# Optimization experiments

Hardware: AMD Instinct MI355X
Metric: run time of the kernel (lower is better)

The kernel has to match this reference:

```python
import jax, jax.numpy as jnp
import numpy as np

D_MODEL = 1024
N_HEADS = 16
D_FF = 4 * D_MODEL
EPS = 1e-5


def _layer_norm(x, g, b):
    mu = jnp.mean(x, axis=-1, keepdims=True)
    var = jnp.mean(jnp.square(x - mu), axis=-1, keepdims=True)
    return (x - mu) * jax.lax.rsqrt(var + EPS) * g + b


def _mha(x, Wq, Wk, Wv, Wo, causal):
    B, S, D = x.shape
    H = N_HEADS
    Dh = D // H
    q = (x @ Wq).reshape(B, S, H, Dh)
    k = (x @ Wk).reshape(B, S, H, Dh)
    v = (x @ Wv).reshape(B, S, H, Dh)
    scores = jnp.einsum('bqhd,bkhd->bhqk', q, k) / jnp.sqrt(jnp.asarray(Dh, x.dtype))
    if causal:
        mask = jnp.tril(jnp.ones((S, S), dtype=bool))  # [S,S] causal mask
        scores = jnp.where(mask, scores, jnp.asarray(-1e9, x.dtype))
    attn = jax.nn.softmax(scores, axis=-1)
    out = jnp.einsum('bhqk,bkhd->bqhd', attn, v).reshape(B, S, D)
    return out @ Wo


def _ffn(x, W1, b1, W2, b2):
    return jax.nn.relu(x @ W1 + b1) @ W2 + b2


def setup_inputs() -> dict:
    key = jax.random.key(0)
    ks = jax.random.split(key, 12)
    sd = 1.0 / np.sqrt(D_MODEL)
    sf = 1.0 / np.sqrt(D_FF)
    B, S = 4, 1024
    return {
        'X': jax.random.normal(ks[0], (B, S, D_MODEL), jnp.float32),
        'Wq1': jax.random.normal(ks[1], (D_MODEL, D_MODEL), jnp.float32) * sd,
        'Wk1': jax.random.normal(ks[2], (D_MODEL, D_MODEL), jnp.float32) * sd,
        'Wv1': jax.random.normal(ks[3], (D_MODEL, D_MODEL), jnp.float32) * sd,
        'Wo1': jax.random.normal(ks[4], (D_MODEL, D_MODEL), jnp.float32) * sd,
        'Wq2': jax.random.normal(ks[5], (D_MODEL, D_MODEL), jnp.float32) * sd,
        'Wk2': jax.random.normal(ks[6], (D_MODEL, D_MODEL), jnp.float32) * sd,
        'Wv2': jax.random.normal(ks[7], (D_MODEL, D_MODEL), jnp.float32) * sd,
        'Wo2': jax.random.normal(ks[8], (D_MODEL, D_MODEL), jnp.float32) * sd,
        'ln_g': jnp.ones((D_MODEL,), jnp.float32),
        'ln_b': jnp.zeros((D_MODEL,), jnp.float32),
        'W1': jax.random.normal(ks[9], (D_MODEL, D_FF), jnp.float32) * sd,
        'b1': jnp.zeros((D_FF,), jnp.float32),
        'W2': jax.random.normal(ks[10], (D_FF, D_MODEL), jnp.float32) * sf,
        'b2': jnp.zeros((D_MODEL,), jnp.float32),
    }


def reference(X, Wq1, Wk1, Wv1, Wo1, Wq2, Wk2, Wv2, Wo2, ln_g, ln_b, W1, b1, W2, b2):
    # Faithful to the torch module (including its unusual residual wiring
    # and the single shared LayerNorm used at all three sites).
    masked = _mha(X, Wq1, Wk1, Wv1, Wo1, causal=True)
    norm_masked = X + _layer_norm(masked, ln_g, ln_b)
    attn2 = _mha(norm_masked, Wq2, Wk2, Wv2, Wo2, causal=False)
    norm_attn2 = attn2 + _layer_norm(attn2, ln_g, ln_b)
    ff = _ffn(norm_attn2, W1, b1, W2, b2)
    return norm_attn2 + _layer_norm(ff, ln_g, ln_b)
```

## Files before the change

### kernel.cpp

```cpp
#include <hip/hip_runtime.h>
#include <hip/hip_bf16.h>

#define D_MODEL 1024
#define N_HEADS 16
#define DH 64
#define D_FF   4096
#define SEQ    1024
#define BATCH  4
#define TOK    (BATCH*SEQ)
#define EPS    1e-5f
#define SCALE  0.125f
#define QSCL   0.18033688f

typedef unsigned short USHORT;
typedef __attribute__((ext_vector_type(8))) short short8v;
typedef __attribute__((ext_vector_type(4))) float f32x4;

__device__ __forceinline__ USHORT f2bf(float f) {
    unsigned int u; __builtin_memcpy(&u, &f, 4);
    u += 0x7fffu + ((u >> 16) & 1u);
    return (USHORT)(u >> 16);
}
__device__ __forceinline__ USHORT f2bf_fast(float f) {
    unsigned int u; __builtin_memcpy(&u, &f, 4);
    return (USHORT)((u + 0x8000u) >> 16);
}
__device__ __forceinline__ float bf2f(USHORT s) {
    unsigned int u = ((unsigned int)s) << 16;
    float f; __builtin_memcpy(&f, &u, 4);
    return f;
}
__device__ __forceinline__ float max3f(float a, float b, float c) {
    return fmaxf(fmaxf(a, b), c);
}

__device__ __forceinline__ short8v ld_frag(const USHORT* lds, int row, int c8) {
    return *reinterpret_cast<const short8v*>(
        &lds[row * 64 + (((c8) ^ (row & 7)) << 3)]);
}
__device__ __forceinline__ short8v ld128(const USHORT* lds, int row, int cu) {
    return *reinterpret_cast<const short8v*>(
        &lds[row * 128 + (((cu) ^ (row & 15)) << 3)]);
}

#define GLDS(gsrc, ldst) \
    __builtin_amdgcn_global_load_lds( \
        (const __attribute__((address_space(1))) void*)(gsrc), \
        (__attribute__((address_space(3))) void*)(ldst), 16, 0, 0)

#define WAITVM(n) asm volatile("s_waitcnt vmcnt(" #n ")" ::: "memory")

__global__ __launch_bounds__(512) void gemm_k256_kernel(
    const USHORT* __restrict__ A, const USHORT* __restrict__ Bt,
    float* __restrict__ Cf, USHORT* __restrict__ Cb, USHORT* __restrict__ Ck,
    USHORT* __restrict__ VtOut,
    int M, int N, int K, const float* __restrict__ bias, int relu, int qkv)
{
    __shared__ USHORT As[2][256 * 64];
    __shared__ USHORT Bs[2][256 * 64];

    const int tid = threadIdx.x;
    const int l   = tid & 63;
    const int w   = tid >> 6;
    const int wr  = w >> 2, wc = w & 3;
    const int lr  = l & 15, lg = l >> 4;

    const int gx  = gridDim.x;
    const int nwg = gx * gridDim.y;
    const int lin = blockIdx.y * gx + blockIdx.x;
    const int swz = (lin & 7) * (nwg >> 3) + (lin >> 3);
    const int m0  = (swz / gx) * 256, n0 = (swz % gx) * 256;

    const USHORT* aS[4]; const USHORT* bS[4]; int dOf[4];
#pragma unroll
    for (int p = 0; p < 4; ++p) {
        const int q = p * 512 + tid;
        const int row = q >> 3, cu = q & 7;
        const int cs = ((cu ^ (row & 7)) << 3);
        aS[p] = A  + (size_t)(m0 + row) * K + cs;
        bS[p] = Bt + (size_t)(n0 + row) * K + cs;
        dOf[p] = (p * 512 + w * 64) * 8;
    }

    auto stage = [&](int buf, int k0) {
#pragma unroll
        for (int p = 0; p < 4; ++p) {
            GLDS(aS[p] + k0, &As[buf][dOf[p]]);
            GLDS(bS[p] + k0, &Bs[buf][dOf[p]]);
        }
    };

    f32x4 acc[8][4];
#pragma unroll
    for (int i = 0; i < 8; ++i)
#pragma unroll
        for (int j = 0; j < 4; ++j) acc[i][j] = (f32x4){0.f, 0.f, 0.f, 0.f};

    const int nk = K >> 6;
    stage(0, 0);

    for (int t = 0; t < nk; ++t) {
        const int cur = t & 1;
        if (t + 1 < nk) {
            stage(cur ^ 1, (t + 1) << 6);
            WAITVM(8);
        } else {
            WAITVM(0);
        }
        __builtin_amdgcn_s_barrier();

#pragma unroll
        for (int ks = 0; ks < 2; ++ks) {
            short8v bfr[4];
#pragma unroll
            for (int ni = 0; ni < 4; ++ni)
                bfr[ni] = ld_frag(Bs[cur], wc * 64 + ni * 16 + lr, ks * 4 + lg);
            __builtin_amdgcn_s_setprio(1);
#pragma unroll
            for (int mi = 0; mi < 8; ++mi) {
                short8v af = ld_frag(As[cur], wr * 128 + mi * 16 + lr, ks * 4 + lg);
#pragma unroll
                for (int ni = 0; ni < 4; ++ni)
                    acc[mi][ni] = __builtin_amdgcn_mfma_f32_16x16x32_bf16(
                        af, bfr[ni], acc[mi][ni], 0, 0, 0);
            }
            __builtin_amdgcn_s_setprio(0);
        }
        __builtin_amdgcn_s_barrier();
    }

    if (qkv) {
#pragma unroll
        for (int mi = 0; mi < 8; ++mi) {
            const int row = m0 + wr * 128 + mi * 16 + (l >> 4) * 4;
#pragma unroll
            for (int ni = 0; ni < 4; ++ni) {
                const int col = n0 + wc * 64 + ni * 16 + lr;
                if (col < 2048) {
                    USHORT* dst = (col < 1024) ? Cb : Ck;
                    const float scl = (col < 1024) ? QSCL : 1.f;
                    const int c = col & 1023;
#pragma unroll
                    for (int j = 0; j < 4; ++j)
                        dst[(size_t)(row + j) * D_MODEL + c] =
                            f2bf(acc[mi][ni][j] * scl);
                } else {
                    const int c = col - 2048;
                    const int bb = row >> 10, jr = row & 1023;
                    const int hh = c >> 6, dd = c & 63;
                    ushort4 pk = make_ushort4(
                        f2bf(acc[mi][ni][0]), f2bf(acc[mi][ni][1]),
                        f2bf(acc[mi][ni][2]), f2bf(acc[mi][ni][3]));
                    *reinterpret_cast<ushort4*>(
                        &VtOut[((size_t)(bb * 16 + hh) * 64 + dd) * 1024 + jr]) = pk;
                }
            }
        }
    } else {
#pragma unroll
        for (int mi = 0; mi < 8; ++mi) {
            const int row = m0 + wr * 128 + mi * 16 + (l >> 4) * 4;
#pragma unroll
            for (int ni = 0; ni < 4; ++ni) {
                const int col = n0 + wc * 64 + ni * 16 + lr;
                const float bv = bias ? bias[col] : 0.f;
#pragma unroll
                for (int j = 0; j < 4; ++j) {
                    float v = acc[mi][ni][j] + bv;
                    if (relu) v = fmaxf(v, 0.f);
                    const size_t idx = (size_t)(row + j) * N + col;
                    if (Cf) Cf[idx] = v;
                    if (Cb) Cb[idx] = f2bf(v);
                }
            }
        }
    }
}

__global__ __launch_bounds__(512) void gemm_k128c_kernel(
    const USHORT* __restrict__ A, const USHORT* __restrict__ Bt,
    USHORT* __restrict__ Pa, USHORT* __restrict__ Pb,
    int M, int N, int K)
{
    __shared__ USHORT As[2][128 * 64];
    __shared__ USHORT Bs[2][128 * 64];

    const int tid = threadIdx.x;
    const int l   = tid & 63;
    const int w   = tid >> 6;
    const int wr  = w >> 2, wc = w & 3;
    const int lr  = l & 15, lg = l >> 4;

    const int gx  = gridDim.x;
    const int nwg = gx * gridDim.y;
    const int lin = blockIdx.y * gx + blockIdx.x;
    const int swz = (lin & 7) * (nwg >> 3) + (lin >> 3);
    const int my  = swz / gx;
    const int mt  = M >> 7;
    const int part = my / mt;
    const int m0  = (my % mt) << 7;
    const int n0  = (swz % gx) * 128;
    const int koff = part * (K >> 1);
    USHORT* dst = part ? Pb : Pa;

    const USHORT* aS[2]; const USHORT* bS[2]; int dOf[2];
#pragma unroll
    for (int p = 0; p < 2; ++p) {
        const int q = p * 512 + tid;
        const int row = q >> 3, cu = q & 7;
        const int cs = ((cu ^ (row & 7)) << 3);
        aS[p] = A  + (size_t)(m0 + row) * K + cs;
        bS[p] = Bt + (size_t)(n0 + row) * K + cs;
        dOf[p] = (p * 512 + w * 64) * 8;
    }

    auto stage = [&](int buf, int k0) {
#pragma unroll
        for (int p = 0; p < 2; ++p) {
            GLDS(aS[p] + k0, &As[buf][dOf[p]]);
            GLDS(bS[p] + k0, &Bs[buf][dOf[p]]);
        }
    };

    f32x4 acc[4][2];
#pragma unroll
    for (int i = 0; i < 4; ++i)
#pragma unroll
        for (int j = 0; j < 2; ++j) acc[i][j] = (f32x4){0.f, 0.f, 0.f, 0.f};

    const int nk = K >> 7;
    stage(0, koff);

    for (int t = 0; t < nk; ++t) {
        const int cur = t & 1;
        if (t + 1 < nk) {
            stage(cur ^ 1, koff + ((t + 1) << 6));
            WAITVM(4);
        } else {
            WAITVM(0);
        }
        __builtin_amdgcn_s_barrier();

#pragma unroll
        for (int ks = 0; ks < 2; ++ks) {
            short8v bfr[2];
#pragma unroll
            for (int ni = 0; ni < 2; ++ni)
                bfr[ni] = ld_frag(Bs[cur], wc * 32 + ni * 16 + lr, ks * 4 + lg);
            __builtin_amdgcn_s_setprio(1);
#pragma unroll
            for (int mi = 0; mi < 4; ++mi) {
                short8v af = ld_frag(As[cur], wr * 64 + mi * 16 + lr, ks * 4 + lg);
#pragma unroll
                for (int ni = 0; ni < 2; ++ni)
                    acc[mi][ni] = __builtin_amdgcn_mfma_f32_16x16x32_bf16(
                        af, bfr[ni], acc[mi][ni], 0, 0, 0);
            }
            __builtin_amdgcn_s_setprio(0);
        }
        __builtin_amdgcn_s_barrier();
    }

#pragma unroll
    for (int mi = 0; mi < 4; ++mi) {
        const int row = m0 + wr * 64 + mi * 16 + (l >> 4) * 4;
#pragma unroll
        for (int ni = 0; ni < 2; ++ni) {
            const int col = n0 + wc * 32 + ni * 16 + lr;
#pragma unroll
            for (int j = 0; j < 4; ++j)
                dst[(size_t)(row + j) * N + col] = f2bf(acc[mi][ni][j]);
        }
    }
}

struct TcvtB4 {
    const float* s0; const float* s1; const float* s2; const float* s3;
    USHORT* d0; USHORT* d1; USHORT* d2; USHORT* d3;
};

__device__ __forceinline__ void tcvt_body(
    const float* __restrict__ W, USHORT* __restrict__ Wt, int K, int N)
{
    __shared__ USHORT L[64][65];
    const int tid = threadIdx.x;
    const int tx = tid & 15, ty = tid >> 4;
    const int n0 = blockIdx.x * 64, k0 = blockIdx.y * 64;
#pragma unroll
    for (int r = 0; r < 4; ++r) {
        int kr = ty + 16 * r;
        float4 v = *reinterpret_cast<const float4*>(
            &W[(size_t)(k0 + kr) * N + n0 + tx * 4]);
        L[tx * 4 + 0][kr] = f2bf(v.x);
        L[tx * 4 + 1][kr] = f2bf(v.y);
        L[tx * 4 + 2][kr] = f2bf(v.z);
        L[tx * 4 + 3][kr] = f2bf(v.w);
    }
    __syncthreads();
#pragma unroll
    for (int r = 0; r < 4; ++r) {
        int nr = ty + 16 * r;
        ushort4 o = make_ushort4(L[nr][tx * 4 + 0], L[nr][tx * 4 + 1],
                                 L[nr][tx * 4 + 2], L[nr][tx * 4 + 3]);
        *reinterpret_cast<ushort4*>(&Wt[(size_t)(n0 + nr) * K + k0 + tx * 4]) = o;
    }
}

__global__ __launch_bounds__(256) void tcvt_kernel(
    const float* __restrict__ W, USHORT* __restrict__ Wt, int K, int N)
{
    tcvt_body(W, Wt, K, N);
}

__global__ __launch_bounds__(256) void tcvt4_kernel(TcvtB4 p, int K, int N)
{
    const int z = blockIdx.z;
    const float* W = (z == 0) ? p.s0 : (z == 1) ? p.s1 : (z == 2) ? p.s2 : p.s3;
    USHORT*    Wt = (z == 0) ? p.d0 : (z == 1) ? p.d1 : (z == 2) ? p.d2 : p.d3;
    tcvt_body(W, Wt, K, N);
}

__global__ __launch_bounds__(256) void f2b_kernel(
    const float* __restrict__ in, USHORT* __restrict__ out, int n4)
{
    int i = blockIdx.x * 256 + threadIdx.x;
    if (i < n4) {
        float4 v = reinterpret_cast<const float4*>(in)[i];
        reinterpret_cast<ushort4*>(out)[i] =
            make_ushort4(f2bf(v.x), f2bf(v.y), f2bf(v.z), f2bf(v.w));
    }
}

__global__ __launch_bounds__(256) void attn_mfma_kernel(
    const USHORT* __restrict__ Q, const USHORT* __restrict__ K,
    const USHORT* __restrict__ Vt, USHORT* __restrict__ O, int causal)
{
    __shared__ USHORT smem[40960];

    const int tid = threadIdx.x;
    const int l  = tid & 63;
    const int w  = tid >> 6;
    const int lr = l & 15;
    const int lg = l >> 4;

    const int lin = blockIdx.y * 16 + blockIdx.x;
    const int swz = (lin & 7) * 128 + (lin >> 3);
    const int qt = swz & 15;
    const int bh = swz >> 4;
    const int h = bh & 15, b = bh >> 4;
    const int q0 = qt * 64;

    const USHORT* gq  = Q  + (size_t)(b * SEQ + q0) * D_MODEL + h * DH;
    const USHORT* gk0 = K  + (size_t)b * SEQ * D_MODEL + h * DH;
    const USHORT* gv0 = Vt + (size_t)bh * DH * SEQ;

    auto stageK = [&](int buf, int kt) {
        USHORT* dst = smem + buf * 8192;
        const size_t base = (size_t)kt * 128 * 1024;
#pragma unroll
        for (int p = 0; p < 4; ++p) {
            const int q = p * 256 + tid;
            const int row = q >> 3, cu = q & 7;
            GLDS(gk0 + base + (size_t)row * 1024 + ((cu ^ (row & 7)) << 3),
                 dst + (p * 256 + w * 64) * 8);
        }
    };
    auto stageV = [&](int buf, int kt) {
        USHORT* dst = smem + 16384 + buf * 8192;
        const int j0 = kt * 128;
#pragma unroll
        for (int p = 0; p < 4; ++p) {
            const int q = p * 256 + tid;
            const int row = q >> 4, cu = q & 15;
            GLDS(gv0 + (size_t)row * 1024 + j0 + ((cu ^ (row & 15)) << 3),
                 dst + (p * 256 + w * 64) * 8);
        }
    };

#pragma unroll
    for (int p = 0; p < 2; ++p) {
        const int q = p * 256 + tid;
        const int row = q >> 3, cu = q & 7;
        GLDS(gq + (size_t)row * 1024 + ((cu ^ (row & 7)) << 3),
             smem + 32768 + (p * 256 + w * 64) * 8);
    }
    stageK(0, 0);
    stageV(0, 0);

    f32x4 oacc[4];
    float m_[4], l_[4];
#pragma unroll
    for (int r = 0; r < 4; ++r) { m_[r] = -1e30f; l_[r] = 0.f; }
#pragma unroll
    for (int d = 0; d < 4; ++d) oacc[d] = (f32x4){0.f, 0.f, 0.f, 0.f};

    int paddr[4][8];
#pragma unroll
    for (int r = 0; r < 4; ++r) {
        const int row = lg * 4 + r;
#pragma unroll
        for (int jb = 0; jb < 8; ++jb) {
            const int cu = jb * 2 + (lr >> 3);
            paddr[r][jb] = row * 128 + ((cu ^ row) << 3) + (lr & 7);
        }
    }

    __syncthreads();
    short8v qa0 = ld_frag(smem + 32768, w * 16 + lr, lg);
    short8v qa1 = ld_frag(smem + 32768, w * 16 + lr, 4 + lg);
    __syncthreads();
    USHORT* PsW = smem + 32768 + w * 2048;

    const int ntile = causal ? (qt >> 1) + 1 : (SEQ / 128);
    for (int kt = 0; kt < ntile; ++kt) {
        const int cur = kt & 1;
        if (kt + 1 < ntile) {
            stageK(cur ^ 1, kt + 1);
            stageV(cur ^ 1, kt + 1);
        }
        const int j0 = kt * 128;
        const USHORT* KsC = smem + cur * 8192;
        const USHORT* VsC = smem + 16384 + cur * 8192;

        f32x4 sa[8];
        __builtin_amdgcn_s_setprio(1);
#pragma unroll
        for (int jb = 0; jb < 8; ++jb) {
            sa[jb] = (f32x4){0.f, 0.f, 0.f, 0.f};
            sa[jb] = __builtin_amdgcn_mfma_f32_16x16x32_bf16(
                qa0, ld_frag(KsC, jb * 16 + lr, lg), sa[jb], 0, 0, 0);
            sa[jb] = __builtin_amdgcn_mfma_f32_16x16x32_bf16(
                qa1, ld_frag(KsC, jb * 16 + lr, 4 + lg), sa[jb], 0, 0, 0);
        }
        __builtin_amdgcn_s_setprio(0);

        if (causal && kt == ntile - 1) {
#pragma unroll
            for (int jb = 0; jb < 8; ++jb)
#pragma unroll
                for (int r = 0; r < 4; ++r)
                    if ((j0 + jb * 16 + lr) > (q0 + w * 16 + lg * 4 + r))
                        sa[jb][r] = -1e30f;
        }

        float tmloc[4];
#pragma unroll
        for (int r = 0; r < 4; ++r)
            tmloc[r] = max3f(max3f(sa[0][r], sa[1][r], sa[2][r]),
                             max3f(sa[3][r], sa[4][r], sa[5][r]),
                             fmaxf(sa[6][r], sa[7][r]));

        const bool anyf = (tmloc[0] > m_[0] + 8.f) | (tmloc[1] > m_[1] + 8.f) |
                          (tmloc[2] > m_[2] + 8.f) | (tmloc[3] > m_[3] + 8.f);
        const unsigned long long bal = __ballot(anyf);
        if ((bal >> (lg * 16)) & 0xFFFFull) {
#pragma unroll
            for (int r = 0; r < 4; ++r) {
                float tm = tmloc[r];
                tm = fmaxf(tm, __shfl_xor(tm, 1));
                tm = fmaxf(tm, __shfl_xor(tm, 2));
                tm = fmaxf(tm, __shfl_xor(tm, 4));
                tm = fmaxf(tm, __shfl_xor(tm, 8));
                if (tm > m_[r] + 8.f) {
                    float sc = exp2f(m_[r] - tm);
                    l_[r] *= sc;
#pragma unroll
                    for (int d = 0; d < 4; ++d) oacc[d][r] *= sc;
                    m_[r] = tm;
                }
            }
        }

#pragma unroll
        for (int r = 0; r < 4; ++r) {
            float rs_ = 0.f;
#pragma unroll
            for (int jb = 0; jb < 8; ++jb) {
                float p = exp2f(sa[jb][r] - m_[r]);
                sa[jb][r] = p;
                rs_ += p;
            }
            l_[r] += rs_;
        }

#pragma unroll
        for (int jb = 0; jb < 8; ++jb)
#pragma unroll
            for (int r = 0; r < 4; ++r)
                PsW[paddr[r][jb]] = f2bf_fast(sa[jb][r]);

        __builtin_amdgcn_s_setprio(1);
#pragma unroll
        for (int ks = 0; ks < 4; ++ks) {
            short8v pa = ld128(PsW, lr, ks * 4 + lg);
#pragma unroll
            for (int d = 0; d < 4; ++d)
                oacc[d] = __builtin_amdgcn_mfma_f32_16x16x32_bf16(
                    pa, ld128(VsC, d * 16 + lr, ks * 4 + lg), oacc[d], 0, 0, 0);
        }
        __builtin_amdgcn_s_setprio(0);
        __syncthreads();
    }

    USHORT* go = O + (size_t)(b * SEQ + q0 + w * 16) * D_MODEL + h * DH;
#pragma unroll
    for (int r = 0; r < 4; ++r) {
        float lv = l_[r];
        lv += __shfl_xor(lv, 1);
        lv += __shfl_xor(lv, 2);
        lv += __shfl_xor(lv, 4);
        lv += __shfl_xor(lv, 8);
        const float inv = 1.f / lv;
        const int qrow = lg * 4 + r;
#pragma unroll
        for (int d = 0; d < 4; ++d)
            go[(size_t)qrow * D_MODEL + d * 16 + lr] = f2bf_fast(oacc[d][r] * inv);
    }
}

__global__ __launch_bounds__(256) void ln_res_kernel(
    const USHORT* __restrict__ xb, const USHORT* __restrict__ xb2,
    const float* __restrict__ biasx,
    const float* __restrict__ resf, const USHORT* __restrict__ resb,
    const float* __restrict__ g, const float* __restrict__ bta,
    float* __restrict__ outf, USHORT* __restrict__ outb)
{
    __shared__ float red[256];
    __shared__ float s_mu, s_rstd;

    const int row = blockIdx.x;
    const int tid = threadIdx.x;
    ushort4 xv = reinterpret_cast<const ushort4*>(xb + (size_t)row * D_MODEL)[tid];
    float vx = bf2f(xv.x), vy = bf2f(xv.y), vz = bf2f(xv.z), vw = bf2f(xv.w);
    if (xb2) {
        ushort4 x2 = reinterpret_cast<const ushort4*>(
            xb2 + (size_t)row * D_MODEL)[tid];
        vx += bf2f(x2.x); vy += bf2f(x2.y); vz += bf2f(x2.z); vw += bf2f(x2.w);
    }
    if (biasx) {
        float4 bx = reinterpret_cast<const float4*>(biasx)[tid];
        vx += bx.x; vy += bx.y; vz += bx.z; vw += bx.w;
    }

    red[tid] = vx + vy + vz + vw;
    __syncthreads();
    for (int s = 128; s > 0; s >>= 1) {
        if (tid < s) red[tid] += red[tid + s];
        __syncthreads();
    }
    if (tid == 0) s_mu = red[0] * (1.f / D_MODEL);
    __syncthreads();
    const float mu = s_mu;

    float dx = vx - mu, dy = vy - mu, dz = vz - mu, dw = vw - mu;
    red[tid] = dx * dx + dy * dy + dz * dz + dw * dw;
    __syncthreads();
    for (int s = 128; s > 0; s >>= 1) {
        if (tid < s) red[tid] += red[tid + s];
        __syncthreads();
    }
    if (tid == 0) s_rstd = rsqrtf(red[0] * (1.f / D_MODEL) + EPS);
    __syncthreads();
    const float rstd = s_rstd;

    float4 rv;
    if (resf) {
        rv = reinterpret_cast<const float4*>(resf + (size_t)row * D_MODEL)[tid];
    } else if (resb) {
        ushort4 rb = reinterpret_cast<const ushort4*>(
            resb + (size_t)row * D_MODEL)[tid];
        rv = make_float4(bf2f(rb.x), bf2f(rb.y), bf2f(rb.z), bf2f(rb.w));
    } else {
        rv = make_float4(vx, vy, vz, vw);
    }
    float4 gv = reinterpret_cast<const float4*>(g)[tid];
    float4 bv = reinterpret_cast<const float4*>(bta)[tid];

    float4 o;
    o.x = rv.x + dx * rstd * gv.x + bv.x;
    o.y = rv.y + dy * rstd * gv.y + bv.y;
    o.z = rv.z + dz * rstd * gv.z + bv.z;
    o.w = rv.w + dw * rstd * gv.w + bv.w;
    reinterpret_cast<float4*>(outf + (size_t)row * D_MODEL)[tid] = o;
    if (outb)
        reinterpret_cast<ushort4*>(outb + (size_t)row * D_MODEL)[tid] =
            make_ushort4(f2bf(o.x), f2bf(o.y), f2bf(o.z), f2bf(o.w));
}

extern "C" void kernel_launch(void* const* d_in, const int* in_sizes, int n_in,
                              void* d_out, int out_size, void* d_ws, size_t ws_size,
                              hipStream_t stream)
{
    const float* X    = (const float*)d_in[0];
    const float* Wq1  = (const float*)d_in[1];
    const float* Wk1  = (const float*)d_in[2];
    const float* Wv1  = (const float*)d_in[3];
    const float* Wo1  = (const float*)d_in[4];
    const float* Wq2  = (const float*)d_in[5];
    const float* Wk2  = (const float*)d_in[6];
    const float* Wv2  = (const float*)d_in[7];
    const float* Wo2  = (const float*)d_in[8];
    const float* ln_g = (const float*)d_in[9];
    const float* ln_b = (const float*)d_in[10];
    const float* W1   = (const float*)d_in[11];
    const float* b1   = (const float*)d_in[12];
    const float* W2   = (const float*)d_in[13];
    const float* b2   = (const float*)d_in[14];

    const size_t MI = 1024 * 1024;
    USHORT* ws16 = (USHORT*)d_ws;
    USHORT* Wqkv1t = ws16;
    USHORT* scr0   = ws16;
    USHORT* Wo1t   = ws16 + 3 * MI;
    USHORT* Wqkv2t = ws16 + 4 * MI;
    USHORT* Wo2t   = ws16 + 7 * MI;
    USHORT* W2t    = ws16 + 8 * MI;
    USHORT* Xb     = ws16 + 12 * MI;
    USHORT* W1t    = Xb;
    USHORT* qb     = ws16 + 16 * MI;
    USHORT* kb     = ws16 + 20 * MI;
    USHORT* Vtb    = ws16 + 24 * MI;
    USHORT* t0b    = ws16 + 28 * MI;
    USHORT* hb     = qb;
    USHORT* t2b    = ws16 + 32 * MI;
    USHORT* t1b    = ws16 + 36 * MI;
    float*  t2     = (float*)(ws16 + 40 * MI);

    auto gemm256 = [&](const USHORT* A, const USHORT* Bt, float* Cf, USHORT* Cb,
                       int M, int N, int K, const float* bias, int relu) {
        gemm_k256_kernel<<<dim3(N / 256, M / 256), 512, 0, stream>>>(
            A, Bt, Cf, Cb, nullptr, nullptr, M, N, K, bias, relu, 0);
    };
    auto gemm_qkv = [&](const USHORT* A, const USHORT* Bt) {
        gemm_k256_kernel<<<dim3(3072 / 256, TOK / 256), 512, 0, stream>>>(
            A, Bt, nullptr, qb, kb, Vtb, TOK, 3072, D_MODEL, nullptr, 0, 1);
    };
    auto gemm128c = [&](const USHORT* A, const USHORT* Bt, USHORT* Pa, USHORT* Pb,
                        int M, int N, int K) {
        gemm_k128c_kernel<<<dim3(N / 128, (M / 128) * 2), 512, 0, stream>>>(
            A, Bt, Pa, Pb, M, N, K);
    };

    dim3 agrid(SEQ / 64, BATCH * N_HEADS);

    {
        TcvtB4 p1{Wq1, Wk1, Wv1, Wo1,
                  Wqkv1t, Wqkv1t + 1 * MI, Wqkv1t + 2 * MI, Wo1t};
        tcvt4_kernel<<<dim3(16, 16, 4), 256, 0, stream>>>(p1, D_MODEL, D_MODEL);
        TcvtB4 p2{Wq2, Wk2, Wv2, Wo2,
                  Wqkv2t, Wqkv2t + 1 * MI, Wqkv2t + 2 * MI, Wo2t};
        tcvt4_kernel<<<dim3(16, 16, 4), 256, 0, stream>>>(p2, D_MODEL, D_MODEL);
    }
    tcvt_kernel<<<dim3(D_MODEL / 64, D_FF / 64), 256, 0, stream>>>(
        W2, W2t, D_FF, D_MODEL);
    f2b_kernel<<<dim3(4096), 256, 0, stream>>>(X, Xb, TOK * D_MODEL / 4);

    gemm_qkv(Xb, Wqkv1t);
    attn_mfma_kernel<<<agrid, 256, 0, stream>>>(qb, kb, Vtb, t0b, 1);
    gemm128c(t0b, Wo1t, t2b, t1b, TOK, D_MODEL, D_MODEL);
    ln_res_kernel<<<dim3(TOK), 256, 0, stream>>>(t2b, t1b, nullptr, X, nullptr,
                                                 ln_g, ln_b, t2, t2b);
    tcvt_kernel<<<dim3(D_FF / 64, D_MODEL / 64), 256, 0, stream>>>(
        W1, W1t, D_MODEL, D_FF);

    gemm_qkv(t2b, Wqkv2t);
    attn_mfma_kernel<<<agrid, 256, 0, stream>>>(qb, kb, Vtb, t0b, 0);
    gemm128c(t0b, Wo2t, scr0, t1b, TOK, D_MODEL, D_MODEL);
    ln_res_kernel<<<dim3(TOK), 256, 0, stream>>>(scr0, t1b, nullptr,
                                                 nullptr, nullptr,
                                                 ln_g, ln_b, t2, t2b);

    gemm256(t2b, W1t, nullptr, hb, TOK, D_FF, D_MODEL, b1, 1);
    gemm128c(hb, W2t, t2b, t1b, TOK, D_MODEL, D_FF);
    ln_res_kernel<<<dim3(TOK), 256, 0, stream>>>(t2b, t1b, b2, t2, nullptr,
                                                 ln_g, ln_b, (float*)d_out, nullptr);
}
```

Baseline: 345.9 us.

## Transpose QK^T MFMA so each lane owns one query row in attention softmax

Swaps the MFMA operands for the score computation so the result is S^T, letting each lane hold all scores for a single query row. Row max and row sum then need only two cross-lane shuffles instead of four per row, and the running max/sum become scalars per lane. P is written to LDS as packed 64-bit stores of four bf16 values instead of sixteen scalar stores, and the rescale factors are redistributed to the O accumulator layout with shuffles. This cuts shuffle and LDS-store instructions in the softmax, in exchange for extra permutes whenever the running max is rescaled.

```diff
diff --git a/kernel.cpp b/kernel.cpp
--- a/kernel.cpp
+++ b/kernel.cpp
@@ -24,6 +24,13 @@
 __device__ __forceinline__ USHORT f2bf_fast(float f) {
     unsigned int u; __builtin_memcpy(&u, &f, 4);
     return (USHORT)((u + 0x8000u) >> 16);
+}
+__device__ __forceinline__ unsigned pk2bf(float lo, float hi) {
+    unsigned ulo, uhi;
+    __builtin_memcpy(&ulo, &lo, 4);
+    __builtin_memcpy(&uhi, &hi, 4);
+    ulo += 0x8000u; uhi += 0x8000u;
+    return (ulo >> 16) | (uhi & 0xffff0000u);
 }
 __device__ __forceinline__ float bf2f(USHORT s) {
     unsigned int u = ((unsigned int)s) << 16;
@@ -388,21 +395,15 @@
     stageV(0, 0);
 
     f32x4 oacc[4];
-    float m_[4], l_[4];
-#pragma unroll
-    for (int r = 0; r < 4; ++r) { m_[r] = -1e30f; l_[r] = 0.f; }
+    float m_ = -1e30f, l_ = 0.f;
 #pragma unroll
     for (int d = 0; d < 4; ++d) oacc[d] = (f32x4){0.f, 0.f, 0.f, 0.f};
 
-    int paddr[4][8];
-#pragma unroll
-    for (int r = 0; r < 4; ++r) {
-        const int row = lg * 4 + r;
-#pragma unroll
-        for (int jb = 0; jb < 8; ++jb) {
-            const int cu = jb * 2 + (lr >> 3);
-            paddr[r][jb] = row * 128 + ((cu ^ row) << 3) + (lr & 7);
-        }
+    int paddr[8];
+#pragma unroll
+    for (int jb = 0; jb < 8; ++jb) {
+        const int cu = jb * 2 + (lg >> 1);
+        paddr[jb] = lr * 128 + ((cu ^ lr) << 3) + (lg & 1) * 4;
     }
 
     __syncthreads();
@@ -428,9 +429,9 @@
         for (int jb = 0; jb < 8; ++jb) {
             sa[jb] = (f32x4){0.f, 0.f, 0.f, 0.f};
             sa[jb] = __builtin_amdgcn_mfma_f32_16x16x32_bf16(
-                qa0, ld_frag(KsC, jb * 16 + lr, lg), sa[jb], 0, 0, 0);
+                ld_frag(KsC, jb * 16 + lr, lg), qa0, sa[jb], 0, 0, 0);
             sa[jb] = __builtin_amdgcn_mfma_f32_16x16x32_bf16(
-                qa1, ld_frag(KsC, jb * 16 + lr, 4 + lg), sa[jb], 0, 0, 0);
+                ld_frag(KsC, jb * 16 + lr, 4 + lg), qa1, sa[jb], 0, 0, 0);
         }
         __builtin_amdgcn_s_setprio(0);
 
@@ -439,55 +440,48 @@
             for (int jb = 0; jb < 8; ++jb)
 #pragma unroll
                 for (int r = 0; r < 4; ++r)
-                    if ((j0 + jb * 16 + lr) > (q0 + w * 16 + lg * 4 + r))
+                    if ((j0 + jb * 16 + lg * 4 + r) > (q0 + w * 16 + lr))
                         sa[jb][r] = -1e30f;
         }
 
-        float tmloc[4];
-#pragma unroll
-        for (int r = 0; r < 4; ++r)
-            tmloc[r] = max3f(max3f(sa[0][r], sa[1][r], sa[2][r]),
-                             max3f(sa[3][r], sa[4][r], sa[5][r]),
-                             fmaxf(sa[6][r], sa[7][r]));
-
-        const bool anyf = (tmloc[0] > m_[0] + 8.f) | (tmloc[1] > m_[1] + 8.f) |
-                          (tmloc[2] > m_[2] + 8.f) | (tmloc[3] > m_[3] + 8.f);
-        const unsigned long long bal = __ballot(anyf);
-        if ((bal >> (lg * 16)) & 0xFFFFull) {
+        float tm = max3f(
+            max3f(max3f(sa[0][0], sa[0][1], sa[0][2]),
+                  max3f(sa[0][3], sa[1][0], sa[1][1]),
+                  max3f(sa[1][2], sa[1][3], sa[2][0])),
+            max3f(max3f(sa[2][1], sa[2][2], sa[2][3]),
+                  max3f(sa[3][0], sa[3][1], sa[3][2]),
+                  max3f(sa[3][3], sa[4][0], sa[4][1])),
+            max3f(max3f(max3f(sa[4][2], sa[4][3], sa[5][0]),
+                        max3f(sa[5][1], sa[5][2], sa[5][3]),
+                        max3f(sa[6][0], sa[6][1], sa[6][2])),
+                  max3f(sa[6][3], sa[7][0], sa[7][1]),
+                  fmaxf(sa[7][2], sa[7][3])));
+        tm = fmaxf(tm, __shfl_xor(tm, 16));
+        tm = fmaxf(tm, __shfl_xor(tm, 32));
+
+        if (__ballot(tm > m_ + 8.f)) {
+            const float mn = (tm > m_ + 8.f) ? tm : m_;
+            const float sc = exp2f(m_ - mn);
+            l_ *= sc;
+            m_ = mn;
 #pragma unroll
             for (int r = 0; r < 4; ++r) {
-                float tm = tmloc[r];
-                tm = fmaxf(tm, __shfl_xor(tm, 1));
-                tm = fmaxf(tm, __shfl_xor(tm, 2));
-                tm = fmaxf(tm, __shfl_xor(tm, 4));
-                tm = fmaxf(tm, __shfl_xor(tm, 8));
-                if (tm > m_[r] + 8.f) {
-                    float sc = exp2f(m_[r] - tm);
-                    l_[r] *= sc;
-#pragma unroll
-                    for (int d = 0; d < 4; ++d) oacc[d][r] *= sc;
-                    m_[r] = tm;
-                }
+                const float scr = __shfl(sc, (l & 48) | (lg * 4 + r));
+#pragma unroll
+                for (int d = 0; d < 4; ++d) oacc[d][r] *= scr;
             }
         }
 
 #pragma unroll
-        for (int r = 0; r < 4; ++r) {
-            float rs_ = 0.f;
-#pragma unroll
-            for (int jb = 0; jb < 8; ++jb) {
-                float p = exp2f(sa[jb][r] - m_[r]);
-                sa[jb][r] = p;
-                rs_ += p;
-            }
-            l_[r] += rs_;
-        }
-
-#pragma unroll
-        for (int jb = 0; jb < 8; ++jb)
-#pragma unroll
-            for (int r = 0; r < 4; ++r)
-                PsW[paddr[r][jb]] = f2bf_fast(sa[jb][r]);
+        for (int jb = 0; jb < 8; ++jb) {
+            const float p0 = exp2f(sa[jb][0] - m_);
+            const float p1 = exp2f(sa[jb][1] - m_);
+            const float p2 = exp2f(sa[jb][2] - m_);
+            const float p3 = exp2f(sa[jb][3] - m_);
+            l_ += (p0 + p1) + (p2 + p3);
+            *reinterpret_cast<uint2*>(&PsW[paddr[jb]]) =
+                make_uint2(pk2bf(p0, p1), pk2bf(p2, p3));
+        }
 
         __builtin_amdgcn_s_setprio(1);
 #pragma unroll
@@ -502,15 +496,15 @@
         __syncthreads();
     }
 
+    float lv = l_;
+    lv += __shfl_xor(lv, 16);
+    lv += __shfl_xor(lv, 32);
+    const float inv_own = 1.f / lv;
+
     USHORT* go = O + (size_t)(b * SEQ + q0 + w * 16) * D_MODEL + h * DH;
 #pragma unroll
     for (int r = 0; r < 4; ++r) {
-        float lv = l_[r];
-        lv += __shfl_xor(lv, 1);
-        lv += __shfl_xor(lv, 2);
-        lv += __shfl_xor(lv, 4);
-        lv += __shfl_xor(lv, 8);
-        const float inv = 1.f / lv;
+        const float inv = __shfl(inv_own, (l & 48) | (lg * 4 + r));
         const int qrow = lg * 4 + r;
 #pragma unroll
         for (int d = 0; d < 4; ++d)
```

New measurement: 338.1 us. 2.2% less time.
